# Kernel tuning notes

Hardware: AMD Instinct MI355X
Metric: run time of the kernel (lower is better)

Reference implementation:

```python
import jax, jax.numpy as jnp
import numpy as np

OUT = 7          # roi_align output_size
NUM_ANCHORS = 27 # 3 scales x 3 ratios x 3 angles
MAX_PROPOSALS = 100
RPN_STRIDE = 32


def conv2d(x, w, b, stride=1, pad=1):
    y = jax.lax.conv_general_dilated(
        x, w, (stride, stride), [(pad, pad), (pad, pad)],
        dimension_numbers=('NCHW', 'OIHW', 'NCHW'))
    return y + b[None, :, None, None]


def generate_anchors(H, W, stride):
    # matches CustomOrientedRPN.generate_anchors
    sx = np.arange(0, W * stride, stride, dtype=np.float32)
    sy = np.arange(0, H * stride, stride, dtype=np.float32)
    SY, SX = np.meshgrid(sy, sx, indexing='ij')
    shifts = np.stack([SX, SY], axis=-1).reshape(-1, 2)  # [HW,2]
    base = []
    for scale in (32.0, 64.0, 128.0):
        for ratio in (0.5, 1.0, 2.0):
            w = scale * ratio ** 0.5
            h = scale / ratio ** 0.5
            for angle in (0.0, 45.0, 90.0):
                base.append([w, h, angle])
    base = np.array(base, dtype=np.float32)  # [A,3]
    A = base.shape[0]
    anchors = np.concatenate(
        [np.repeat(shifts[:, None, :], A, axis=1),
         np.broadcast_to(base[None], (shifts.shape[0], A, 3))], axis=-1)
    return jnp.asarray(anchors.reshape(-1, 5))  # [HW*A, 5]


def rotated_roi_align(features, boxes, batch_idx):
    # Vectorized version of the per-box affine_grid + grid_sample loop
    # (align_corners=False semantics for both, zero padding for grid_sample).
    B, C, Hf, Wf = features.shape
    lin = (2.0 * jnp.arange(OUT, dtype=features.dtype) + 1.0) / OUT - 1.0
    ys, xs = jnp.meshgrid(lin, lin, indexing='ij')  # [7,7] base grid

    cx, cy, w, h, ang = (boxes[:, i] for i in range(5))
    ar = -ang * jnp.pi / 180.0
    c, s = jnp.cos(ar), jnp.sin(ar)
    t00 = w / Wf * c; t01 = -h / Hf * s; t02 = 2.0 * cx / Wf - 1.0
    t10 = w / Wf * s; t11 = h / Hf * c;  t12 = 2.0 * cy / Hf - 1.0
    gx = t00[:, None, None] * xs + t01[:, None, None] * ys + t02[:, None, None]  # [N,7,7]
    gy = t10[:, None, None] * xs + t11[:, None, None] * ys + t12[:, None, None]

    ix = ((gx + 1.0) * Wf - 1.0) / 2.0
    iy = ((gy + 1.0) * Hf - 1.0) / 2.0
    x0 = jnp.floor(ix); y0 = jnp.floor(iy)
    wx = ix - x0;       wy = iy - y0
    x0i = x0.astype(jnp.int32); y0i = y0.astype(jnp.int32)

    def gather(dx, dy, wgt):
        xi = x0i + dx; yi = y0i + dy
        valid = (xi >= 0) & (xi < Wf) & (yi >= 0) & (yi < Hf)
        xc = jnp.clip(xi, 0, Wf - 1)
        yc = jnp.clip(yi, 0, Hf - 1)
        def one(bi, yb, xb):
            return features[bi][:, yb, xb]  # [C,7,7]
        vals = jax.vmap(one)(batch_idx, yc, xc)  # [N,C,7,7]
        return vals * (wgt * valid)[:, None, :, :]

    return (gather(0, 0, (1 - wx) * (1 - wy)) + gather(1, 0, wx * (1 - wy)) +
            gather(0, 1, (1 - wx) * wy) + gather(1, 1, wx * wy))


def setup_inputs() -> dict:
    key = jax.random.key(0)
    ks = jax.random.split(key, 20)

    def w(k, shape):
        fan_in = int(np.prod(shape[1:]))
        return jax.random.normal(k, shape, jnp.float32) / np.sqrt(fan_in)

    C = 256; A = NUM_ANCHORS; NC = 5
    return {
        'images': jax.random.normal(ks[0], (8, 3, 1024, 1024), jnp.float32),
        'backbone_w': w(ks[1], (C, 3, 3, 3)),   'backbone_b': jnp.zeros((C,), jnp.float32),
        'rpn_conv_w': w(ks[2], (256, C, 3, 3)), 'rpn_conv_b': jnp.zeros((256,), jnp.float32),
        'obj_w': w(ks[3], (A, 256, 1, 1)),      'obj_b': jnp.zeros((A,), jnp.float32),
        'delta_w': w(ks[4], (A * 5, 256, 1, 1)) * 0.1, 'delta_b': jnp.zeros((A * 5,), jnp.float32),
        'fc1_w': w(ks[5], (1024, C * OUT * OUT)), 'fc1_b': jnp.zeros((1024,), jnp.float32),
        'fc2_w': w(ks[6], (1024, 1024)),          'fc2_b': jnp.zeros((1024,), jnp.float32),
        'cls_w': w(ks[7], (NC, 1024)),            'cls_b': jnp.zeros((NC,), jnp.float32),
        'bbox_w': w(ks[8], (5, 1024)),            'bbox_b': jnp.zeros((5,), jnp.float32),
    }


def reference(images, backbone_w, backbone_b, rpn_conv_w, rpn_conv_b,
              obj_w, obj_b, delta_w, delta_b,
              fc1_w, fc1_b, fc2_w, fc2_b, cls_w, cls_b, bbox_w, bbox_b):
    # backbone (stand-in: single stride-16 conv)
    f = conv2d(images, backbone_w, backbone_b, stride=16, pad=1)  # [B,256,64,64]
    B, C, H, W = f.shape
    # F.interpolate(scale_factor=0.5, bilinear, align_corners=False) == 2x2 mean
    f = f.reshape(B, C, H // 2, 2, W // 2, 2).mean(axis=(3, 5))   # [B,256,32,32]
    Hf, Wf = f.shape[2], f.shape[3]

    # RPN
    t = jax.nn.relu(conv2d(f, rpn_conv_w, rpn_conv_b, 1, 1))
    _logits = conv2d(t, obj_w, obj_b, 1, 0)  # computed as in original (unused downstream)
    deltas = conv2d(t, delta_w, delta_b, 1, 0)  # [B, A*5, Hf, Wf]
    A = NUM_ANCHORS
    deltas = deltas.reshape(B, A, 5, Hf, Wf).transpose(0, 3, 4, 1, 2).reshape(B, -1, 5)

    anchors = generate_anchors(Hf, Wf, RPN_STRIDE)  # [HW*A,5]
    acx, acy, aw, ah, aa = (anchors[:, i] for i in range(5))
    pcx = deltas[:, :, 0] * aw + acx
    pcy = deltas[:, :, 1] * ah + acy
    pw = jnp.exp(deltas[:, :, 2]) * aw
    ph = jnp.exp(deltas[:, :, 3]) * ah
    pa = aa + deltas[:, :, 4]
    proposals = jnp.stack([pcx, pcy, pw, ph, pa], axis=-1)  # [B, HW*A, 5]
    proposals = proposals[:, :MAX_PROPOSALS]                # p[:max_proposals]

    boxes = proposals.reshape(-1, 5)                        # [B*100, 5]
    batch_idx = jnp.repeat(jnp.arange(B), MAX_PROPOSALS)
    pooled = rotated_roi_align(f, boxes, batch_idx)         # [B*100, 256, 7, 7]

    x = pooled.reshape(pooled.shape[0], -1)
    x = jax.nn.relu(x @ fc1_w.T + fc1_b)
    x = jax.nn.relu(x @ fc2_w.T + fc2_b)
    class_logits = x @ cls_w.T + cls_b
    obb_preds = x @ bbox_w.T + bbox_b
    return class_logits, obb_preds
```

## Files before the change

kernel.cpp:

```cpp
#include <hip/hip_runtime.h>
#include <hip/hip_bf16.h>

using bf16 = __hip_bfloat16;

typedef __attribute__((ext_vector_type(8))) short bf16x8;
typedef __attribute__((ext_vector_type(4))) float f32x4;

__device__ __forceinline__ void async16(const void* g, void* l) {
  __builtin_amdgcn_global_load_lds(
      (const __attribute__((address_space(1))) unsigned int*)g,
      (__attribute__((address_space(3))) unsigned int*)l, 16, 0, 0);
}

__device__ __forceinline__ void store_o(float* C, size_t i, float v) { C[i] = v; }
__device__ __forceinline__ void store_o(bf16* C, size_t i, float v) {
  C[i] = __float2bfloat16(v);
}

__global__ __launch_bounds__(256) void k_backbone(const float* __restrict__ img,
    const float* __restrict__ w, const float* __restrict__ bias,
    float* __restrict__ f) {
  __shared__ float wlds[6912];
  __shared__ float patch[432];
  int blk = blockIdx.x;
  int xq = blk & 7, y = (blk >> 3) & 31, b = blk >> 8;
  int x0 = xq * 4;
  int t = threadIdx.x;
  for (int i = t; i < 6912; i += 256) wlds[i] = w[i];
  for (int i = t; i < 432; i += 256) {
    int k27 = i % 27, r = i / 27;
    int sub = r & 3, p = r >> 2;
    int kx = k27 % 3, ky = (k27 / 3) % 3, cin = k27 / 9;
    int sy = sub >> 1, sx = sub & 1;
    int iy = (2 * y + sy) * 16 - 1 + ky;
    int ix = (2 * (x0 + p) + sx) * 16 - 1 + kx;
    float v = 0.f;
    if (iy >= 0 && ix >= 0)
      v = img[((size_t)(b * 3 + cin) * 1024 + iy) * 1024 + ix];
    patch[i] = v;
  }
  __syncthreads();
  int c = t;
  float wr[27];
#pragma unroll
  for (int k = 0; k < 27; ++k) wr[k] = wlds[c * 27 + k];
  float bs = bias[c];
#pragma unroll
  for (int p = 0; p < 4; ++p) {
    float acc = 0.f;
#pragma unroll
    for (int sub = 0; sub < 4; ++sub)
#pragma unroll
      for (int k = 0; k < 27; ++k)
        acc += patch[(p * 4 + sub) * 27 + k] * wr[k];
    f[(size_t)((b * 32 + y) * 32 + x0 + p) * 256 + c] = acc * 0.25f + bs;
  }
}

__global__ __launch_bounds__(256) void k_rpn(const float* __restrict__ f,
    const float* __restrict__ rpn_w, float* __restrict__ part) {
  int p = blockIdx.x;
  int kc = blockIdx.y;
  int x = p & 3, b = p >> 2;
  __shared__ float fpl[6][16];
  int tid = threadIdx.x;
  if (tid < 96) {
    int cin2 = tid & 15;
    int rc = tid >> 4;
    int row = rc / 3, col = rc % 3;
    int xc = x - 1 + col;
    float v = 0.f;
    if (xc >= 0)
      v = f[((size_t)(b * 32 + row) * 32 + xc) * 256 + kc * 16 + cin2];
    fpl[rc][cin2] = v;
  }
  __syncthreads();
  int c = tid;
  const float* wbase = rpn_w + (size_t)c * 2304 + kc * 144;
  float acc = 0.f;
#pragma unroll
  for (int cin2 = 0; cin2 < 16; ++cin2) {
    const float* wp = wbase + cin2 * 9;
    acc += fpl[0][cin2] * wp[3] + fpl[1][cin2] * wp[4]
         + fpl[2][cin2] * wp[5] + fpl[3][cin2] * wp[6]
         + fpl[4][cin2] * wp[7] + fpl[5][cin2] * wp[8];
  }
  part[((size_t)kc * 32 + p) * 256 + c] = acc;
}

__global__ __launch_bounds__(512) void k_delta(const float* __restrict__ part,
    const float* __restrict__ rpn_b,
    const float* __restrict__ dw, const float* __restrict__ db,
    float* __restrict__ boxes) {
  int p = blockIdx.x;
  int x = p & 3, b = p >> 2;
  __shared__ float tbuf[256];
  __shared__ float dvals[135];
  int tid = threadIdx.x;
  if (tid < 256) {
    float s = rpn_b[tid];
#pragma unroll
    for (int kc = 0; kc < 16; ++kc)
      s += part[((size_t)kc * 32 + p) * 256 + tid];
    tbuf[tid] = fmaxf(s, 0.f);
  }
  __syncthreads();
  if (tid < 270) {
    int o = tid >> 1, half = tid & 1;
    const float* wp = dw + (size_t)o * 256 + half * 128;
    const float* tp = tbuf + half * 128;
    float s = 0.f;
#pragma unroll 8
    for (int k = 0; k < 128; ++k) s += tp[k] * wp[k];
    s += __shfl_xor(s, 1, 64);
    if (half == 0) dvals[o] = s + db[o];
  }
  __syncthreads();
  if (tid < 27) {
    int i = x * 27 + tid;
    if (i < 100) {
      int a = tid;
      int si = a / 9, ri = (a / 3) % 3, ai = a % 3;
      float scale = 32.f * (float)(1 << si);
      float sr = (ri == 0) ? 0.70710678118654752f : (ri == 1 ? 1.0f : 1.41421356237309505f);
      float aw = scale * sr, ah = scale / sr;
      float aang = 45.f * (float)ai;
      float acx = 32.f * (float)x, acy = 0.f;
      float* bx = boxes + (size_t)(b * 100 + i) * 5;
      bx[0] = dvals[a * 5 + 0] * aw + acx;
      bx[1] = dvals[a * 5 + 1] * ah + acy;
      bx[2] = expf(dvals[a * 5 + 2]) * aw;
      bx[3] = expf(dvals[a * 5 + 3]) * ah;
      bx[4] = aang + dvals[a * 5 + 4];
    }
  }
}

__global__ __launch_bounds__(256) void k_roialign(const float* __restrict__ f,
    const float* __restrict__ boxes, bf16* __restrict__ pooled) {
  int n = blockIdx.x;
  int b = n / 100;
  __shared__ int six[49], siy[49];
  __shared__ float swx[49], swy[49];
  __shared__ float pool_s[12544];
  int tid = threadIdx.x;
  if (tid < 49) {
    float cx = boxes[n * 5 + 0], cy = boxes[n * 5 + 1];
    float w = boxes[n * 5 + 2], h = boxes[n * 5 + 3], ang = boxes[n * 5 + 4];
    float ar = -ang * 0.017453292519943295f;
    float cc = cosf(ar), ss = sinf(ar);
    float t00 = w * (1.f / 32.f) * cc, t01 = -h * (1.f / 32.f) * ss;
    float t02 = cx * (2.f / 32.f) - 1.f;
    float t10 = w * (1.f / 32.f) * ss, t11 = h * (1.f / 32.f) * cc;
    float t12 = cy * (2.f / 32.f) - 1.f;
    int py = tid / 7, px = tid - py * 7;
    float lx = (2.f * px + 1.f) * (1.f / 7.f) - 1.f;
    float ly = (2.f * py + 1.f) * (1.f / 7.f) - 1.f;
    float gx = t00 * lx + t01 * ly + t02;
    float gy = t10 * lx + t11 * ly + t12;
    float ix = ((gx + 1.f) * 32.f - 1.f) * 0.5f;
    float iy = ((gy + 1.f) * 32.f - 1.f) * 0.5f;
    float x0 = floorf(ix), y0 = floorf(iy);
    six[tid] = (int)x0; siy[tid] = (int)y0;
    swx[tid] = ix - x0; swy[tid] = iy - y0;
  }
  __syncthreads();
  const float* fb = f + (size_t)b * 262144;
  int c = tid;
#pragma unroll 7
  for (int bin = 0; bin < 49; ++bin) {
    int x0 = six[bin], y0 = siy[bin];
    float wx = swx[bin], wy = swy[bin];
    bool x0ok = (x0 >= 0) & (x0 < 32), x1ok = (x0 + 1 >= 0) & (x0 + 1 < 32);
    bool y0ok = (y0 >= 0) & (y0 < 32), y1ok = (y0 + 1 >= 0) & (y0 + 1 < 32);
    int x0c = min(max(x0, 0), 31), x1c = min(max(x0 + 1, 0), 31);
    int y0c = min(max(y0, 0), 31), y1c = min(max(y0 + 1, 0), 31);
    float w00 = (x0ok && y0ok) ? (1.f - wx) * (1.f - wy) : 0.f;
    float w01 = (x1ok && y0ok) ? wx * (1.f - wy) : 0.f;
    float w10 = (x0ok && y1ok) ? (1.f - wx) * wy : 0.f;
    float w11 = (x1ok && y1ok) ? wx * wy : 0.f;
    float acc = fb[(y0c * 32 + x0c) * 256 + c] * w00
              + fb[(y0c * 32 + x1c) * 256 + c] * w01
              + fb[(y1c * 32 + x0c) * 256 + c] * w10
              + fb[(y1c * 32 + x1c) * 256 + c] * w11;
    pool_s[c * 49 + bin] = acc;
  }
  __syncthreads();
  bf16* po = pooled + (size_t)n * 12544;
  for (int k = tid; k < 12544; k += 256) po[k] = __float2bfloat16(pool_s[k]);
}

__device__ __forceinline__ unsigned int pk2(float a, float b) {
  unsigned int ua = __bfloat16_as_ushort(__float2bfloat16(a));
  unsigned int ub = __bfloat16_as_ushort(__float2bfloat16(b));
  return ua | (ub << 16);
}
__global__ __launch_bounds__(256) void k_cvtz(const float* __restrict__ s1,
    const float* __restrict__ s2, uint2* __restrict__ d1,
    uint2* __restrict__ d2, f32x4* __restrict__ Pz) {
  const int N1 = 3211264;
  const int N2 = 262144;
  const int NZ = 204800;
  int stride = gridDim.x * 256;
  for (int j = blockIdx.x * 256 + threadIdx.x; j < N1 + N2 + NZ; j += stride) {
    if (j < N1) {
      float4 v = ((const float4*)s1)[j];
      uint2 o; o.x = pk2(v.x, v.y); o.y = pk2(v.z, v.w);
      d1[j] = o;
    } else if (j < N1 + N2) {
      int i = j - N1;
      float4 v = ((const float4*)s2)[i];
      uint2 o; o.x = pk2(v.x, v.y); o.y = pk2(v.z, v.w);
      d2[i] = o;
    } else {
      Pz[j - N1 - N2] = (f32x4){0.f, 0.f, 0.f, 0.f};
    }
  }
}

__global__ __launch_bounds__(256) void k_gemm_bb(
    const unsigned short* __restrict__ A, const unsigned short* __restrict__ B,
    float* __restrict__ P, int M, int N, int K, int KC) {
  int b = blockIdx.x;
  int x8 = b & 7, j = b >> 3;
  int g = j / 56, t2 = j - g * 56;
  int z = x8 + 8 * g;
  int kbeg = z * KC;
  if (kbeg >= K) return;
  int kend = kbeg + KC; if (kend > K) kend = K;
  int n0 = (t2 & 7) * 128;
  int m0 = (t2 >> 3) * 128;

  __shared__ unsigned short As[2][128 * 64];
  __shared__ unsigned short Bs[2][128 * 64];
  int t = threadIdx.x;
  int wv = t >> 6, ln = t & 63;
  int quad = ln >> 4, l15 = ln & 15;
  int wm = wv >> 1, wn = wv & 1;

  int srow = ln >> 3;
  int sg = (ln & 7) ^ srow;
  const unsigned short* Ap[4];
#pragma unroll
  for (int q = 0; q < 4; ++q) {
    int r = m0 + q * 32 + wv * 8 + srow;
    if (r > M - 1) r = M - 1;
    Ap[q] = A + (size_t)r * K + sg * 8;
  }
  const unsigned short* Bp[4];
#pragma unroll
  for (int c = 0; c < 4; ++c) {
    int r = n0 + wv * 32 + c * 8 + srow;
    Bp[c] = B + (size_t)r * K + sg * 8;
  }

  f32x4 acc[4][4];
#pragma unroll
  for (int mf = 0; mf < 4; ++mf)
#pragma unroll
    for (int nf = 0; nf < 4; ++nf) acc[mf][nf] = (f32x4){0.f, 0.f, 0.f, 0.f};

#pragma unroll
  for (int q = 0; q < 4; ++q)
    async16(Ap[q] + kbeg, &As[0][q * 2048 + wv * 512]);
#pragma unroll
  for (int c = 0; c < 4; ++c)
    async16(Bp[c] + kbeg, &Bs[0][wv * 2048 + c * 512]);

  int cur = 0;
  for (int k0 = kbeg; k0 < kend; k0 += 64) {
    int k1 = k0 + 64;
    if (k1 < kend) {
#pragma unroll
      for (int q = 0; q < 4; ++q)
        async16(Ap[q] + k1, &As[cur ^ 1][q * 2048 + wv * 512]);
#pragma unroll
      for (int c = 0; c < 4; ++c)
        async16(Bp[c] + k1, &Bs[cur ^ 1][wv * 2048 + c * 512]);
      asm volatile("s_waitcnt vmcnt(8)" ::: "memory");
    } else {
      asm volatile("s_waitcnt vmcnt(0)" ::: "memory");
    }
    __builtin_amdgcn_s_barrier();
    __builtin_amdgcn_sched_barrier(0);
#pragma unroll
    for (int ks = 0; ks < 2; ++ks) {
      bf16x8 a[4];
#pragma unroll
      for (int mf = 0; mf < 4; ++mf) {
        int row = wm * 64 + mf * 16 + l15;
        a[mf] = *(const bf16x8*)&As[cur][row * 64 + (((ks * 4 + quad) ^ (l15 & 7)) * 8)];
      }
#pragma unroll
      for (int nf = 0; nf < 4; ++nf) {
        int brow = wn * 64 + nf * 16 + l15;
        bf16x8 b2 = *(const bf16x8*)&Bs[cur][brow * 64 + (((ks * 4 + quad) ^ (l15 & 7)) * 8)];
#pragma unroll
        for (int mf = 0; mf < 4; ++mf)
          acc[mf][nf] = __builtin_amdgcn_mfma_f32_16x16x32_bf16(a[mf], b2, acc[mf][nf], 0, 0, 0);
      }
    }
    __builtin_amdgcn_sched_barrier(0);
    asm volatile("" ::: "memory");
    __builtin_amdgcn_s_barrier();
    cur ^= 1;
  }
#pragma unroll
  for (int nf = 0; nf < 4; ++nf) {
    int n = n0 + wn * 64 + nf * 16 + l15;
#pragma unroll
    for (int mf = 0; mf < 4; ++mf) {
#pragma unroll
      for (int r = 0; r < 4; ++r) {
        int m = m0 + wm * 64 + mf * 16 + quad * 4 + r;
        if (m < M) atomicAdd(&P[(size_t)m * N + n], acc[mf][nf][r]);
      }
    }
  }
}

template <typename OutT, bool RZ>
__global__ __launch_bounds__(256) void k_bias_relu(float* __restrict__ P,
    const float* __restrict__ bias, OutT* __restrict__ C, int MN, int N) {
  int i = blockIdx.x * 256 + threadIdx.x;
  if (i * 4 >= MN) return;
  f32x4 s = *(const f32x4*)(P + (size_t)i * 4);
  int n = (i * 4) % N;
#pragma unroll
  for (int u = 0; u < 4; ++u)
    store_o(C, (size_t)i * 4 + u, fmaxf(s[u] + bias[n + u], 0.f));
  if (RZ) *(f32x4*)(P + (size_t)i * 4) = (f32x4){0.f, 0.f, 0.f, 0.f};
}

__global__ __launch_bounds__(640) void k_heads(const float* __restrict__ x2,
    const float* __restrict__ cls_w, const float* __restrict__ cls_b,
    const float* __restrict__ bbox_w, const float* __restrict__ bbox_b,
    float* __restrict__ out) {
  int n = blockIdx.x;
  int wave = threadIdx.x >> 6;
  int lane = threadIdx.x & 63;
  const float* w = (wave < 5) ? (cls_w + (size_t)wave * 1024)
                              : (bbox_w + (size_t)(wave - 5) * 1024);
  const float* xr = x2 + (size_t)n * 1024;
  float s = 0.f;
  for (int k = lane; k < 1024; k += 64) s += xr[k] * w[k];
  for (int off = 32; off; off >>= 1) s += __shfl_down(s, off, 64);
  if (lane == 0) {
    int o = (wave < 5) ? wave : wave - 5;
    float bias = (wave < 5) ? cls_b[o] : bbox_b[o];
    int base = (wave < 5) ? 0 : 4000;
    out[base + n * 5 + o] = s + bias;
  }
}

extern "C" void kernel_launch(void* const* d_in, const int* in_sizes, int n_in,
                              void* d_out, int out_size, void* d_ws, size_t ws_size,
                              hipStream_t stream) {
  const float* images     = (const float*)d_in[0];
  const float* backbone_w = (const float*)d_in[1];
  const float* backbone_b = (const float*)d_in[2];
  const float* rpn_w      = (const float*)d_in[3];
  const float* rpn_b      = (const float*)d_in[4];
  const float* delta_w    = (const float*)d_in[7];
  const float* delta_b    = (const float*)d_in[8];
  const float* fc1_w      = (const float*)d_in[9];
  const float* fc1_b      = (const float*)d_in[10];
  const float* fc2_w      = (const float*)d_in[11];
  const float* fc2_b      = (const float*)d_in[12];
  const float* cls_w      = (const float*)d_in[13];
  const float* cls_b      = (const float*)d_in[14];
  const float* bbox_w     = (const float*)d_in[15];
  const float* bbox_b     = (const float*)d_in[16];

  char* ws = (char*)d_ws;
  bf16*  bw1    = (bf16*) ws;
  float* f      = (float*)ws;
  float* boxes  = (float*)(ws + 25690112);
  bf16*  pooled = (bf16*) (ws + 25706496);
  float* x2     = (float*)(ws + 25706496);
  bf16*  x1     = (bf16*) (ws + 45776896);
  float* P      = (float*)(ws + 47415296);
  bf16*  bw2    = (bf16*) (ws + 50692096);
  float* rpart  = P;

  k_backbone<<<2048, 256, 0, stream>>>(images, backbone_w, backbone_b, f);
  k_rpn<<<dim3(32, 16), 256, 0, stream>>>(f, rpn_w, rpart);
  k_delta<<<32, 512, 0, stream>>>(rpart, rpn_b, delta_w, delta_b, boxes);
  k_roialign<<<800, 256, 0, stream>>>(f, boxes, pooled);

  k_cvtz<<<2048, 256, 0, stream>>>(fc1_w, fc2_w, (uint2*)bw1, (uint2*)bw2,
                                   (f32x4*)P);

  k_gemm_bb<<<896, 256, 0, stream>>>(
      (const unsigned short*)pooled, (const unsigned short*)bw1, P,
      800, 1024, 12544, 896);
  k_bias_relu<bf16, true><<<800, 256, 0, stream>>>(P, fc1_b, x1, 819200, 1024);

  k_gemm_bb<<<448, 256, 0, stream>>>(
      (const unsigned short*)x1, (const unsigned short*)bw2, P,
      800, 1024, 1024, 128);
  k_bias_relu<float, false><<<800, 256, 0, stream>>>(P, fc2_b, x2, 819200, 1024);

  k_heads<<<800, 640, 0, stream>>>(x2, cls_w, cls_b, bbox_w, bbox_b, (float*)d_out);
}
```

Before: 357.8 us.

## Fuse fc2 bias-relu into heads, split fc1 GEMM launch, vectorize pooled stores

```diff
diff --git a/kernel.cpp b/kernel.cpp
--- a/kernel.cpp
+++ b/kernel.cpp
@@ -15,6 +15,12 @@
 __device__ __forceinline__ void store_o(float* C, size_t i, float v) { C[i] = v; }
 __device__ __forceinline__ void store_o(bf16* C, size_t i, float v) {
   C[i] = __float2bfloat16(v);
+}
+
+__device__ __forceinline__ unsigned int pk2(float a, float b) {
+  unsigned int ua = __bfloat16_as_ushort(__float2bfloat16(a));
+  unsigned int ub = __bfloat16_as_ushort(__float2bfloat16(b));
+  return ua | (ub << 16);
 }
 
 __global__ __launch_bounds__(256) void k_backbone(const float* __restrict__ img,
@@ -109,9 +115,15 @@
     int o = tid >> 1, half = tid & 1;
     const float* wp = dw + (size_t)o * 256 + half * 128;
     const float* tp = tbuf + half * 128;
-    float s = 0.f;
+    float s0 = 0.f, s1 = 0.f, s2 = 0.f, s3 = 0.f;
 #pragma unroll 8
-    for (int k = 0; k < 128; ++k) s += tp[k] * wp[k];
+    for (int k = 0; k < 128; k += 4) {
+      s0 += tp[k]     * wp[k];
+      s1 += tp[k + 1] * wp[k + 1];
+      s2 += tp[k + 2] * wp[k + 2];
+      s3 += tp[k + 3] * wp[k + 3];
+    }
+    float s = (s0 + s1) + (s2 + s3);
     s += __shfl_xor(s, 1, 64);
     if (half == 0) dvals[o] = s + db[o];
   }
@@ -186,15 +198,14 @@
     pool_s[c * 49 + bin] = acc;
   }
   __syncthreads();
-  bf16* po = pooled + (size_t)n * 12544;
-  for (int k = tid; k < 12544; k += 256) po[k] = __float2bfloat16(pool_s[k]);
-}
-
-__device__ __forceinline__ unsigned int pk2(float a, float b) {
-  unsigned int ua = __bfloat16_as_ushort(__float2bfloat16(a));
-  unsigned int ub = __bfloat16_as_ushort(__float2bfloat16(b));
-  return ua | (ub << 16);
-}
+  uint2* po = (uint2*)(pooled + (size_t)n * 12544);
+  for (int k = tid; k < 3136; k += 256) {
+    f32x4 v = *(const f32x4*)&pool_s[k * 4];
+    uint2 o; o.x = pk2(v[0], v[1]); o.y = pk2(v[2], v[3]);
+    po[k] = o;
+  }
+}
+
 __global__ __launch_bounds__(256) void k_cvtz(const float* __restrict__ s1,
     const float* __restrict__ s2, uint2* __restrict__ d1,
     uint2* __restrict__ d2, f32x4* __restrict__ Pz) {
@@ -220,11 +231,10 @@
 
 __global__ __launch_bounds__(256) void k_gemm_bb(
     const unsigned short* __restrict__ A, const unsigned short* __restrict__ B,
-    float* __restrict__ P, int M, int N, int K, int KC) {
+    float* __restrict__ P, int M, int N, int K, int KC, int zmul, int zoff) {
   int b = blockIdx.x;
-  int x8 = b & 7, j = b >> 3;
-  int g = j / 56, t2 = j - g * 56;
-  int z = x8 + 8 * g;
+  int xcd = b & 7, t2 = b >> 3;
+  int z = zmul * xcd + zoff;
   int kbeg = z * KC;
   if (kbeg >= K) return;
   int kend = kbeg + KC; if (kend > K) kend = K;
@@ -332,16 +342,20 @@
   if (RZ) *(f32x4*)(P + (size_t)i * 4) = (f32x4){0.f, 0.f, 0.f, 0.f};
 }
 
-__global__ __launch_bounds__(640) void k_heads(const float* __restrict__ x2,
+__global__ __launch_bounds__(640) void k_heads(const float* __restrict__ P,
+    const float* __restrict__ fc2_b,
     const float* __restrict__ cls_w, const float* __restrict__ cls_b,
     const float* __restrict__ bbox_w, const float* __restrict__ bbox_b,
     float* __restrict__ out) {
+  __shared__ float xr[1024];
   int n = blockIdx.x;
+  for (int i = threadIdx.x; i < 1024; i += 640)
+    xr[i] = fmaxf(P[(size_t)n * 1024 + i] + fc2_b[i], 0.f);
+  __syncthreads();
   int wave = threadIdx.x >> 6;
   int lane = threadIdx.x & 63;
   const float* w = (wave < 5) ? (cls_w + (size_t)wave * 1024)
                               : (bbox_w + (size_t)(wave - 5) * 1024);
-  const float* xr = x2 + (size_t)n * 1024;
   float s = 0.f;
   for (int k = lane; k < 1024; k += 64) s += xr[k] * w[k];
   for (int off = 32; off; off >>= 1) s += __shfl_down(s, off, 64);
@@ -377,7 +391,6 @@
   float* f      = (float*)ws;
   float* boxes  = (float*)(ws + 25690112);
   bf16*  pooled = (bf16*) (ws + 25706496);
-  float* x2     = (float*)(ws + 25706496);
   bf16*  x1     = (bf16*) (ws + 45776896);
   float* P      = (float*)(ws + 47415296);
   bf16*  bw2    = (bf16*) (ws + 50692096);
@@ -391,15 +404,18 @@
   k_cvtz<<<2048, 256, 0, stream>>>(fc1_w, fc2_w, (uint2*)bw1, (uint2*)bw2,
                                    (f32x4*)P);
 
-  k_gemm_bb<<<896, 256, 0, stream>>>(
+  k_gemm_bb<<<448, 256, 0, stream>>>(
       (const unsigned short*)pooled, (const unsigned short*)bw1, P,
-      800, 1024, 12544, 896);
+      800, 1024, 12544, 896, 2, 0);
+  k_gemm_bb<<<448, 256, 0, stream>>>(
+      (const unsigned short*)pooled, (const unsigned short*)bw1, P,
+      800, 1024, 12544, 896, 2, 1);
   k_bias_relu<bf16, true><<<800, 256, 0, stream>>>(P, fc1_b, x1, 819200, 1024);
 
   k_gemm_bb<<<448, 256, 0, stream>>>(
       (const unsigned short*)x1, (const unsigned short*)bw2, P,
-      800, 1024, 1024, 128);
-  k_bias_relu<float, false><<<800, 256, 0, stream>>>(P, fc2_b, x2, 819200, 1024);
-
-  k_heads<<<800, 640, 0, stream>>>(x2, cls_w, cls_b, bbox_w, bbox_b, (float*)d_out);
-}
+      800, 1024, 1024, 128, 1, 0);
+
+  k_heads<<<800, 640, 0, stream>>>(P, fc2_b, cls_w, cls_b, bbox_w, bbox_b,
+                                   (float*)d_out);
+}
```

Result: no change. 357.0 us (-0.2%).
